# Kernel tuning notes

Hardware: AMD Instinct MI355X
Metric: run time of the kernel (lower is better)

Reference implementation:

```python
import jax, jax.numpy as jnp
import numpy as np

B, S, DIM = 8, 1, 2048
H = 16
QLR, KVLR = 1536, 512
DN, DR, DV = 128, 64, 128      # qk_nope, qk_rope, v head dims
START = 8191                    # start_pos; end_pos = START + S = 8192
EPS = 1e-6
SCALE = (DN + DR) ** -0.5


def _rms(x, w):
    # F.rms_norm: x / sqrt(mean(x^2)+eps) * w
    return x * w * jax.lax.rsqrt(jnp.mean(jnp.square(x), axis=-1, keepdims=True) + EPS)


def _rope(x, cos, sin):
    # x: [..., r]; consecutive pairs (x0,x1) treated as complex, multiplied by cos+i*sin
    xr, xi = x[..., 0::2], x[..., 1::2]
    out_r = xr * cos - xi * sin
    out_i = xr * sin + xi * cos
    return jnp.stack([out_r, out_i], axis=-1).reshape(x.shape)


def setup_inputs() -> dict:
    key = jax.random.key(0)
    ks = jax.random.split(key, 12)
    # rotary tables for the single decode position
    inv_freq = 1.0 / (10000.0 ** (np.arange(0, DR, 2, dtype=np.float32) / DR))  # [DR/2]
    pos = np.arange(START, START + S, dtype=np.float32)[:, None]                # [S,1]
    ang = pos * inv_freq[None, :]                                               # [S, DR/2]
    return {
        "x": jax.random.normal(ks[0], (B, S, DIM), jnp.float32),
        "start_pos": START,
        "freqs_cos": jnp.asarray(np.cos(ang)),
        "freqs_sin": jnp.asarray(np.sin(ang)),
        "kv_cache_prefix": jax.random.normal(ks[1], (B, START, KVLR), jnp.float32),
        "pe_cache_prefix": jax.random.normal(ks[2], (B, START, DR), jnp.float32),
        "wq_a_w": jax.random.normal(ks[3], (QLR, DIM), jnp.float32) * 0.02,
        "wq_a_b": jnp.zeros((QLR,), jnp.float32),
        "q_norm_w": jnp.ones((QLR,), jnp.float32),
        "wq_b_w": jax.random.normal(ks[4], (H * (DN + DR), QLR), jnp.float32) * 0.02,
        "wq_b_b": jnp.zeros((H * (DN + DR),), jnp.float32),
        "wkv_a_w": jax.random.normal(ks[5], (KVLR + DR, DIM), jnp.float32) * 0.02,
        "wkv_a_b": jnp.zeros((KVLR + DR,), jnp.float32),
        "kv_norm_w": jnp.ones((KVLR,), jnp.float32),
        "wkv_b_w": jax.random.normal(ks[6], (H * (DN + DV), KVLR), jnp.float32) * 0.02,
        "wo_w": jax.random.normal(ks[7], (DIM, H * DV), jnp.float32) * 0.02,
        "wo_b": jnp.zeros((DIM,), jnp.float32),
    }


def reference(x, start_pos, freqs_cos, freqs_sin, kv_cache_prefix, pe_cache_prefix,
              wq_a_w, wq_a_b, q_norm_w, wq_b_w, wq_b_b,
              wkv_a_w, wkv_a_b, kv_norm_w, wkv_b_w, wo_w, wo_b):
    b, s, _ = x.shape
    # low-rank query projection
    q = _rms(x @ wq_a_w.T + wq_a_b, q_norm_w) @ wq_b_w.T + wq_b_b
    q = q.reshape(b, s, H, DN + DR)
    q_nope, q_pe = q[..., :DN], q[..., DN:]
    cos = freqs_cos[None, :, None, :]  # [1,s,1,DR/2]
    sin = freqs_sin[None, :, None, :]
    q_pe = _rope(q_pe, cos, sin)
    # compressed KV + rope key branch
    kvpe = x @ wkv_a_w.T + wkv_a_b               # [b,s,KVLR+DR]
    kv, k_pe = kvpe[..., :KVLR], kvpe[..., KVLR:]
    k_pe = _rope(k_pe[:, :, None, :], cos, sin)[:, :, 0, :]
    # weight absorption: project q_nope into latent space through wkv_b's K-part
    wkv_b = wkv_b_w.reshape(H, DN + DV, KVLR)
    q_abs = jnp.einsum('bshd,hdc->bshc', q_nope, wkv_b[:, :DN])
    # append current step to caches
    kv_cache = jnp.concatenate([kv_cache_prefix, _rms(kv, kv_norm_w)], axis=1)  # [b,t,KVLR]
    pe_cache = jnp.concatenate([pe_cache_prefix, k_pe], axis=1)                 # [b,t,DR]
    # attention in latent space (seqlen=1 decode -> no causal mask needed)
    scores = (jnp.einsum('bshc,btc->bsht', q_abs, kv_cache)
              + jnp.einsum('bshr,btr->bsht', q_pe, pe_cache)) * SCALE
    attn = jax.nn.softmax(scores.astype(jnp.float32), axis=-1).astype(x.dtype)
    out = jnp.einsum('bsht,btc->bshc', attn, kv_cache)
    out = jnp.einsum('bshc,hdc->bshd', out, wkv_b[:, DN:])  # V-part of wkv_b
    return out.reshape(b, s, H * DV) @ wo_w.T + wo_b
```

## Files before the change

### kernel.cpp

```cpp
#include <hip/hip_runtime.h>
#include <math.h>

namespace {
constexpr int B_   = 8;
constexpr int DIM_ = 2048;
constexpr int H_   = 16;
constexpr int QLR_ = 1536;
constexpr int KVLR_= 512;
constexpr int DN_  = 128;
constexpr int DR_  = 64;
constexpr int DV_  = 128;
constexpr int TPRE_= 8191;
constexpr int CE_  = 576;
constexpr int NCH_ = 32;
constexpr int CT_  = 256;
constexpr float EPS_ = 1e-6f;
constexpr float SCALE_ = 0.07216878364870322f;
constexpr int SSTR_ = 20;

constexpr size_t WS_QLAT  = 0;
constexpr size_t WS_KVPE  = WS_QLAT  + (size_t)B_*QLR_;
constexpr size_t WS_KVNEW = WS_KVPE  + (size_t)B_*CE_;
constexpr size_t WS_PENEW = WS_KVNEW + (size_t)B_*KVLR_;
constexpr size_t WS_QRS   = WS_PENEW + (size_t)B_*DR_;
constexpr size_t WS_QNOPE = WS_QRS   + (size_t)B_;
constexpr size_t WS_QT    = WS_QNOPE + (size_t)B_*H_*DN_;
constexpr size_t WS_MLOC  = WS_QT    + (size_t)B_*CE_*H_;
constexpr size_t WS_LLOC  = WS_MLOC  + (size_t)B_*H_*NCH_;
constexpr size_t WS_OUT2  = WS_LLOC  + (size_t)B_*H_*NCH_;
constexpr size_t WS_OPART = WS_OUT2  + (size_t)B_*DIM_;
}

__global__ __launch_bounds__(256) void mla_k1(const float* __restrict__ x,
                                              const float* __restrict__ wqa,
                                              const float* __restrict__ bqa,
                                              const float* __restrict__ wkva,
                                              const float* __restrict__ bkva,
                                              float* __restrict__ ws) {
  const int w = threadIdx.x >> 6, l = threadIdx.x & 63;
  const int r = blockIdx.x * 4 + w;
  const float* W; const float* bias; float* out; int rr; int ostride;
  if (r < QLR_) { W = wqa;  bias = bqa;  out = ws + WS_QLAT; rr = r;        ostride = QLR_; }
  else          { W = wkva; bias = bkva; out = ws + WS_KVPE; rr = r - QLR_; ostride = CE_;  }
  const float4* wp = (const float4*)(W + (size_t)rr * DIM_);
  const float4* x4 = (const float4*)x;
  float4 wv[8];
#pragma unroll
  for (int j = 0; j < 8; ++j) wv[j] = wp[l + 64 * j];
  float acc[B_];
#pragma unroll
  for (int b = 0; b < B_; ++b) acc[b] = 0.f;
#pragma unroll
  for (int b = 0; b < B_; ++b) {
#pragma unroll
    for (int j = 0; j < 8; ++j) {
      const float4 xv = x4[b * (DIM_ / 4) + l + 64 * j];
      acc[b] = fmaf(wv[j].x, xv.x, fmaf(wv[j].y, xv.y, fmaf(wv[j].z, xv.z, fmaf(wv[j].w, xv.w, acc[b]))));
    }
  }
#pragma unroll
  for (int b = 0; b < B_; ++b)
#pragma unroll
    for (int s = 32; s; s >>= 1) acc[b] += __shfl_xor(acc[b], s);
  if (l == 0) {
    const float b0 = bias[rr];
#pragma unroll
    for (int b = 0; b < B_; ++b) out[b * ostride + rr] = acc[b] + b0;
  }
}

__global__ __launch_bounds__(256) void mla_k2(const float* __restrict__ kvnw,
                                              const float* __restrict__ fcos,
                                              const float* __restrict__ fsin,
                                              float* __restrict__ ws) {
  const int tid = threadIdx.x;
  const int b = tid >> 5, i = tid & 31;
  const float* kvpe = ws + WS_KVPE + b * CE_;
  float ss = 0.f;
#pragma unroll
  for (int j = 0; j < KVLR_ / 32; ++j) { const float v = kvpe[i + 32 * j]; ss = fmaf(v, v, ss); }
#pragma unroll
  for (int s = 16; s; s >>= 1) ss += __shfl_xor(ss, s, 32);
  const float scale = 1.0f / sqrtf(ss / (float)KVLR_ + EPS_);
  float* kvn = ws + WS_KVNEW + b * KVLR_;
#pragma unroll
  for (int j = 0; j < KVLR_ / 32; ++j) {
    const int c = i + 32 * j;
    kvn[c] = kvpe[c] * kvnw[c] * scale;
  }
  {
    const float xr = kvpe[KVLR_ + 2 * i], xi = kvpe[KVLR_ + 2 * i + 1];
    const float c = fcos[i], s = fsin[i];
    float* pen = ws + WS_PENEW + b * DR_;
    pen[2 * i]     = xr * c - xi * s;
    pen[2 * i + 1] = xr * s + xi * c;
  }
  {
    const float* p = ws + WS_QLAT + b * QLR_;
    float sq = 0.f;
#pragma unroll
    for (int j = 0; j < QLR_ / 32; ++j) { const float v = p[i + 32 * j]; sq = fmaf(v, v, sq); }
#pragma unroll
    for (int s = 16; s; s >>= 1) sq += __shfl_xor(sq, s, 32);
    if (i == 0) ws[WS_QRS + b] = 1.0f / sqrtf(sq / (float)QLR_ + EPS_);
  }
}

__global__ __launch_bounds__(256) void mla_k3(const float* __restrict__ qnw,
                                              const float* __restrict__ wqb,
                                              const float* __restrict__ bqb,
                                              const float* __restrict__ fcos,
                                              const float* __restrict__ fsin,
                                              float* __restrict__ ws) {
  const int w = threadIdx.x >> 6, l = threadIdx.x & 63;
  const int r0 = blockIdx.x * 8 + w * 2;
  const float4* w0p = (const float4*)(wqb + (size_t)r0 * QLR_);
  const float4* w1p = (const float4*)(wqb + (size_t)(r0 + 1) * QLR_);
  const float4* g4  = (const float4*)qnw;
  const float4* x4  = (const float4*)(ws + WS_QLAT);
  float4 wg0[6], wg1[6];
#pragma unroll
  for (int j = 0; j < 6; ++j) {
    const int c4 = l + 64 * j;
    const float4 a = w0p[c4], bb = w1p[c4], g = g4[c4];
    wg0[j].x = a.x * g.x; wg0[j].y = a.y * g.y; wg0[j].z = a.z * g.z; wg0[j].w = a.w * g.w;
    wg1[j].x = bb.x * g.x; wg1[j].y = bb.y * g.y; wg1[j].z = bb.z * g.z; wg1[j].w = bb.w * g.w;
  }
  float acc0[B_], acc1[B_];
#pragma unroll
  for (int b = 0; b < B_; ++b) { acc0[b] = 0.f; acc1[b] = 0.f; }
#pragma unroll
  for (int b = 0; b < B_; ++b) {
#pragma unroll
    for (int j = 0; j < 6; ++j) {
      const float4 xv = x4[b * (QLR_ / 4) + l + 64 * j];
      acc0[b] = fmaf(wg0[j].x, xv.x, fmaf(wg0[j].y, xv.y, fmaf(wg0[j].z, xv.z, fmaf(wg0[j].w, xv.w, acc0[b]))));
      acc1[b] = fmaf(wg1[j].x, xv.x, fmaf(wg1[j].y, xv.y, fmaf(wg1[j].z, xv.z, fmaf(wg1[j].w, xv.w, acc1[b]))));
    }
  }
#pragma unroll
  for (int b = 0; b < B_; ++b)
#pragma unroll
    for (int s = 32; s; s >>= 1) {
      acc0[b] += __shfl_xor(acc0[b], s);
      acc1[b] += __shfl_xor(acc1[b], s);
    }
  if (l == 0) {
    const int h = r0 / (DN_ + DR_);
    const int j0 = r0 - h * (DN_ + DR_);
    const float b0 = bqb[r0], b1 = bqb[r0 + 1];
    if (j0 < DN_) {
      float* qn = ws + WS_QNOPE;
#pragma unroll
      for (int b = 0; b < B_; ++b) {
        const float sb = ws[WS_QRS + b];
        qn[(b * H_ + h) * DN_ + j0]     = acc0[b] * sb + b0;
        qn[(b * H_ + h) * DN_ + j0 + 1] = acc1[b] * sb + b1;
      }
    } else {
      const int i = (j0 - DN_) >> 1;
      const float c = fcos[i], s = fsin[i];
      float* qT = ws + WS_QT;
#pragma unroll
      for (int b = 0; b < B_; ++b) {
        const float sb = ws[WS_QRS + b];
        const float xr = acc0[b] * sb + b0, xi = acc1[b] * sb + b1;
        qT[((size_t)b * CE_ + KVLR_ + 2 * i) * H_ + h]     = xr * c - xi * s;
        qT[((size_t)b * CE_ + KVLR_ + 2 * i + 1) * H_ + h] = xr * s + xi * c;
      }
    }
  }
}

__global__ __launch_bounds__(256) void mla_k4(const float* __restrict__ wkvb,
                                              float* __restrict__ ws) {
  __shared__ float red[7 * 32 * B_];
  const int h = blockIdx.y;
  const int strip = blockIdx.x;
  const int tid = threadIdx.x;
  const int c = tid & 31, dg = tid >> 5;
  const int cg = strip * 32 + c;
  const float* qn = ws + WS_QNOPE;
  float acc[B_];
#pragma unroll
  for (int b = 0; b < B_; ++b) acc[b] = 0.f;
  const float* wp = wkvb + (size_t)h * 256 * KVLR_ + cg;
#pragma unroll
  for (int dd = 0; dd < 16; ++dd) {
    const int d = dg * 16 + dd;
    const float wv = wp[(size_t)d * KVLR_];
#pragma unroll
    for (int b = 0; b < B_; ++b) acc[b] = fmaf(qn[(b * H_ + h) * DN_ + d], wv, acc[b]);
  }
  if (dg > 0) {
#pragma unroll
    for (int b = 0; b < B_; ++b) red[(((dg - 1) * 32) + c) * B_ + b] = acc[b];
  }
  __syncthreads();
  if (dg == 0) {
    float* qT = ws + WS_QT;
#pragma unroll
    for (int b = 0; b < B_; ++b) {
      float v = acc[b];
#pragma unroll
      for (int g = 0; g < 7; ++g) v += red[(g * 32 + c) * B_ + b];
      qT[((size_t)b * CE_ + cg) * H_ + h] = v;
    }
  }
}

__global__ __launch_bounds__(256) void mla_k5(const float* __restrict__ kvpre,
                                              const float* __restrict__ pepre,
                                              float* __restrict__ ws) {
  __shared__ float sl[CT_ * SSTR_];
  const int b = blockIdx.y;
  const int chunk = blockIdx.x;
  const int t0 = chunk * CT_;
  const int tid = threadIdx.x;
  const int w = tid >> 6, l = tid & 63;
  const float* kvnew = ws + WS_KVNEW;
  const float* penew = ws + WS_PENEW;

  {
    const int t = t0 + (w << 6) + l;
    const float* kvrow; const float* perow;
    if (t < TPRE_) {
      kvrow = kvpre + ((size_t)b * TPRE_ + t) * KVLR_;
      perow = pepre + ((size_t)b * TPRE_ + t) * DR_;
    } else {
      kvrow = kvnew + b * KVLR_;
      perow = penew + b * DR_;
    }
    const float* qTb = ws + WS_QT + (size_t)b * CE_ * H_;
    float acc[H_];
#pragma unroll
    for (int h = 0; h < H_; ++h) acc[h] = 0.f;
    auto fma4 = [&](const float4 k, const float* qc) {
#pragma unroll
      for (int h = 0; h < H_; ++h) {
        acc[h] = fmaf(qc[h],          k.x, acc[h]);
        acc[h] = fmaf(qc[H_ + h],     k.y, acc[h]);
        acc[h] = fmaf(qc[2 * H_ + h], k.z, acc[h]);
        acc[h] = fmaf(qc[3 * H_ + h], k.w, acc[h]);
      }
    };
    for (int c16 = 0; c16 < KVLR_; c16 += 16) {
      const float4 k0 = *(const float4*)(kvrow + c16);
      const float4 k1 = *(const float4*)(kvrow + c16 + 4);
      const float4 k2 = *(const float4*)(kvrow + c16 + 8);
      const float4 k3 = *(const float4*)(kvrow + c16 + 12);
      const float* qc = qTb + (size_t)c16 * H_;
      fma4(k0, qc);
      fma4(k1, qc + 4 * H_);
      fma4(k2, qc + 8 * H_);
      fma4(k3, qc + 12 * H_);
    }
    {
      const float4 k0 = *(const float4*)(perow);
      const float4 k1 = *(const float4*)(perow + 4);
      const float4 k2 = *(const float4*)(perow + 8);
      const float4 k3 = *(const float4*)(perow + 12);
      const float4 k4 = *(const float4*)(perow + 16);
      const float4 k5 = *(const float4*)(perow + 20);
      const float4 k6 = *(const float4*)(perow + 24);
      const float4 k7 = *(const float4*)(perow + 28);
      const float* qc = qTb + (size_t)KVLR_ * H_;
      fma4(k0, qc);            fma4(k1, qc + 4 * H_);
      fma4(k2, qc + 8 * H_);   fma4(k3, qc + 12 * H_);
      fma4(k4, qc + 16 * H_);  fma4(k5, qc + 20 * H_);
      fma4(k6, qc + 24 * H_);  fma4(k7, qc + 28 * H_);
      const float4 k8 = *(const float4*)(perow + 32);
      const float4 k9 = *(const float4*)(perow + 36);
      const float4 ka = *(const float4*)(perow + 40);
      const float4 kb = *(const float4*)(perow + 44);
      const float4 kc = *(const float4*)(perow + 48);
      const float4 kd = *(const float4*)(perow + 52);
      const float4 ke = *(const float4*)(perow + 56);
      const float4 kf = *(const float4*)(perow + 60);
      fma4(k8, qc + 32 * H_);  fma4(k9, qc + 36 * H_);
      fma4(ka, qc + 40 * H_);  fma4(kb, qc + 44 * H_);
      fma4(kc, qc + 48 * H_);  fma4(kd, qc + 52 * H_);
      fma4(ke, qc + 56 * H_);  fma4(kf, qc + 60 * H_);
    }
    const int tl = (w << 6) + l;
#pragma unroll
    for (int g = 0; g < 4; ++g) {
      float4 v;
      v.x = acc[4 * g] * SCALE_; v.y = acc[4 * g + 1] * SCALE_;
      v.z = acc[4 * g + 2] * SCALE_; v.w = acc[4 * g + 3] * SCALE_;
      *(float4*)(sl + tl * SSTR_ + 4 * g) = v;
    }
  }
  __syncthreads();

  {
    const int h2 = tid >> 4, grp = tid & 15;
    float m = -3.4e38f;
#pragma unroll
    for (int j = 0; j < 16; ++j) m = fmaxf(m, sl[(grp + 16 * j) * SSTR_ + h2]);
#pragma unroll
    for (int s = 8; s; s >>= 1) m = fmaxf(m, __shfl_xor(m, s, 16));
    float lsum = 0.f;
#pragma unroll
    for (int j = 0; j < 16; ++j) {
      const int idx = (grp + 16 * j) * SSTR_ + h2;
      const float p = __expf(sl[idx] - m);
      sl[idx] = p;
      lsum += p;
    }
#pragma unroll
    for (int s = 8; s; s >>= 1) lsum += __shfl_xor(lsum, s, 16);
    if (grp == 0) {
      ws[WS_MLOC + (b * H_ + h2) * NCH_ + chunk] = m;
      ws[WS_LLOC + (b * H_ + h2) * NCH_ + chunk] = lsum;
    }
  }
  __syncthreads();

  {
    float o[4][8];
#pragma unroll
    for (int a = 0; a < 4; ++a)
#pragma unroll
      for (int j = 0; j < 8; ++j) o[a][j] = 0.f;
    const int hb = w * 4;
    const float* kvb = kvpre + (size_t)b * TPRE_ * KVLR_;
    auto step = [&](const float* kr, int t) {
      const float4 p = *(const float4*)(sl + t * SSTR_ + hb);
#pragma unroll
      for (int j = 0; j < 4; ++j) {
        const float2 kv = *(const float2*)(kr + j * 128 + 2 * l);
        o[0][2 * j]     = fmaf(p.x, kv.x, o[0][2 * j]);
        o[0][2 * j + 1] = fmaf(p.x, kv.y, o[0][2 * j + 1]);
        o[1][2 * j]     = fmaf(p.y, kv.x, o[1][2 * j]);
        o[1][2 * j + 1] = fmaf(p.y, kv.y, o[1][2 * j + 1]);
        o[2][2 * j]     = fmaf(p.z, kv.x, o[2][2 * j]);
        o[2][2 * j + 1] = fmaf(p.z, kv.y, o[2][2 * j + 1]);
        o[3][2 * j]     = fmaf(p.w, kv.x, o[3][2 * j]);
        o[3][2 * j + 1] = fmaf(p.w, kv.y, o[3][2 * j + 1]);
      }
    };
    if (t0 + CT_ <= TPRE_) {
#pragma unroll 4
      for (int t = 0; t < CT_; ++t) step(kvb + (size_t)(t0 + t) * KVLR_, t);
    } else {
      const float* kvn = kvnew + b * KVLR_;
      for (int t = 0; t < CT_; ++t) {
        const float* kr = (t0 + t < TPRE_) ? (kvb + (size_t)(t0 + t) * KVLR_) : kvn;
        step(kr, t);
      }
    }
    float* Op = ws + WS_OPART;
#pragma unroll
    for (int a = 0; a < 4; ++a) {
#pragma unroll
      for (int j = 0; j < 4; ++j) {
        float2 v; v.x = o[a][2 * j]; v.y = o[a][2 * j + 1];
        *(float2*)(Op + (((size_t)(b * H_ + hb + a) * NCH_ + chunk) * KVLR_) + j * 128 + 2 * l) = v;
      }
    }
  }
}

__global__ __launch_bounds__(256) void mla_k6(const float* __restrict__ wkvb,
                                              float* __restrict__ ws) {
  const int h = blockIdx.x, b = blockIdx.y;
  __shared__ float wgt[NCH_];
  __shared__ float ao[KVLR_];
  __shared__ float Linv;
  const int tid = threadIdx.x;
  if (tid < NCH_) {
    const float m = ws[WS_MLOC + (b * H_ + h) * NCH_ + tid];
    float M = m;
#pragma unroll
    for (int s = 16; s; s >>= 1) M = fmaxf(M, __shfl_xor(M, s, 32));
    const float wv = __expf(m - M);
    wgt[tid] = wv;
    float lv = ws[WS_LLOC + (b * H_ + h) * NCH_ + tid] * wv;
#pragma unroll
    for (int s = 16; s; s >>= 1) lv += __shfl_xor(lv, s, 32);
    if (tid == 0) Linv = 1.0f / lv;
  }
  __syncthreads();
  const float* Ob = ws + WS_OPART + (size_t)(b * H_ + h) * NCH_ * KVLR_;
  float s0 = 0.f, s1 = 0.f;
#pragma unroll 4
  for (int i = 0; i < NCH_; ++i) {
    const float wv = wgt[i];
    s0 = fmaf(wv, Ob[(size_t)i * KVLR_ + tid], s0);
    s1 = fmaf(wv, Ob[(size_t)i * KVLR_ + tid + 256], s1);
  }
  const float li = Linv;
  ao[tid] = s0 * li;
  ao[tid + 256] = s1 * li;
  __syncthreads();
  const int v = tid >> 1, half = tid & 1;
  const float* w2 = wkvb + ((size_t)h * 256 + DN_ + v) * KVLR_ + half * 256;
  const float* a = ao + half * 256;
  float s = 0.f;
#pragma unroll
  for (int c = 0; c < 256; c += 4) {
    const float4 wv = *(const float4*)(w2 + c);
    s = fmaf(wv.x, a[c], s);
    s = fmaf(wv.y, a[c + 1], s);
    s = fmaf(wv.z, a[c + 2], s);
    s = fmaf(wv.w, a[c + 3], s);
  }
  s += __shfl_xor(s, 1);
  if (half == 0) ws[WS_OUT2 + b * DIM_ + h * DV_ + v] = s;
}

__global__ __launch_bounds__(256) void mla_k7(const float* __restrict__ wo,
                                              const float* __restrict__ wob,
                                              const float* __restrict__ ws,
                                              float* __restrict__ out) {
  const int w = threadIdx.x >> 6, l = threadIdx.x & 63;
  const int r = blockIdx.x * 4 + w;
  const float4* wp = (const float4*)(wo + (size_t)r * DIM_);
  const float4* x4 = (const float4*)(ws + WS_OUT2);
  float4 wv[8];
#pragma unroll
  for (int j = 0; j < 8; ++j) wv[j] = wp[l + 64 * j];
  float acc[B_];
#pragma unroll
  for (int b = 0; b < B_; ++b) acc[b] = 0.f;
#pragma unroll
  for (int b = 0; b < B_; ++b) {
#pragma unroll
    for (int j = 0; j < 8; ++j) {
      const float4 xv = x4[b * (DIM_ / 4) + l + 64 * j];
      acc[b] = fmaf(wv[j].x, xv.x, fmaf(wv[j].y, xv.y, fmaf(wv[j].z, xv.z, fmaf(wv[j].w, xv.w, acc[b]))));
    }
  }
#pragma unroll
  for (int b = 0; b < B_; ++b)
#pragma unroll
    for (int s = 32; s; s >>= 1) acc[b] += __shfl_xor(acc[b], s);
  if (l == 0) {
    const float b0 = wob[r];
#pragma unroll
    for (int b = 0; b < B_; ++b) out[b * DIM_ + r] = acc[b] + b0;
  }
}

extern "C" void kernel_launch(void* const* d_in, const int* in_sizes, int n_in,
                              void* d_out, int out_size, void* d_ws, size_t ws_size,
                              hipStream_t stream) {
  (void)in_sizes; (void)n_in; (void)out_size; (void)ws_size;
  const float* x     = (const float*)d_in[0];
  const float* fcos  = (const float*)d_in[2];
  const float* fsin  = (const float*)d_in[3];
  const float* kvpre = (const float*)d_in[4];
  const float* pepre = (const float*)d_in[5];
  const float* wqa   = (const float*)d_in[6];
  const float* bqa   = (const float*)d_in[7];
  const float* qnw   = (const float*)d_in[8];
  const float* wqb   = (const float*)d_in[9];
  const float* bqb   = (const float*)d_in[10];
  const float* wkva  = (const float*)d_in[11];
  const float* bkva  = (const float*)d_in[12];
  const float* kvnw  = (const float*)d_in[13];
  const float* wkvb  = (const float*)d_in[14];
  const float* wo    = (const float*)d_in[15];
  const float* wob   = (const float*)d_in[16];
  float* ws  = (float*)d_ws;
  float* out = (float*)d_out;

  mla_k1<<<dim3((QLR_ + CE_) / 4), dim3(256), 0, stream>>>(x, wqa, bqa, wkva, bkva, ws);
  mla_k2<<<dim3(1), dim3(256), 0, stream>>>(kvnw, fcos, fsin, ws);
  mla_k3<<<dim3(H_ * (DN_ + DR_) / 8), dim3(256), 0, stream>>>(qnw, wqb, bqb, fcos, fsin, ws);
  mla_k4<<<dim3(16, H_), dim3(256), 0, stream>>>(wkvb, ws);
  mla_k5<<<dim3(NCH_, B_), dim3(256), 0, stream>>>(kvpre, pepre, ws);
  mla_k6<<<dim3(H_, B_), dim3(256), 0, stream>>>(wkvb, ws);
  mla_k7<<<dim3(DIM_ / 4), dim3(256), 0, stream>>>(wo, wob, ws, out);
}
```

Measured before the change: 408.8 us.

## Split attention chunks smaller and parallelize score dot-products across four warps

Chunk count doubles to 64 with 128 tokens each, and mla_k5 moves to 512 threads. Four wave-pairs each compute a slice of the 576-wide score dot product per token, and the partial sums are reduced through shared memory. Each wave now accumulates two heads in the PV stage instead of four. The goal is more blocks and more parallelism per token, giving better occupancy and latency hiding on the bandwidth-bound cache scan. The cost is extra shared-memory traffic, one more barrier, and twice the partial-output writes and reads in mla_k6.

```diff
diff --git a/kernel.cpp b/kernel.cpp
--- a/kernel.cpp
+++ b/kernel.cpp
@@ -12,8 +12,8 @@
 constexpr int DV_  = 128;
 constexpr int TPRE_= 8191;
 constexpr int CE_  = 576;
-constexpr int NCH_ = 32;
-constexpr int CT_  = 256;
+constexpr int NCH_ = 64;
+constexpr int CT_  = 128;
 constexpr float EPS_ = 1e-6f;
 constexpr float SCALE_ = 0.07216878364870322f;
 constexpr int SSTR_ = 20;
@@ -209,9 +209,10 @@
   }
 }
 
-__global__ __launch_bounds__(256) void mla_k5(const float* __restrict__ kvpre,
-                                              const float* __restrict__ pepre,
-                                              float* __restrict__ ws) {
+__global__ __launch_bounds__(512, 4) void mla_k5(const float* __restrict__ kvpre,
+                                                 const float* __restrict__ pepre,
+                                                 float* __restrict__ ws) {
+  __shared__ float part[4 * CT_ * SSTR_];
   __shared__ float sl[CT_ * SSTR_];
   const int b = blockIdx.y;
   const int chunk = blockIdx.x;
@@ -222,7 +223,9 @@
   const float* penew = ws + WS_PENEW;
 
   {
-    const int t = t0 + (w << 6) + l;
+    const int q4 = w >> 1;
+    const int tl = ((w & 1) << 6) + l;
+    const int t = t0 + tl;
     const float* kvrow; const float* perow;
     if (t < TPRE_) {
       kvrow = kvpre + ((size_t)b * TPRE_ + t) * KVLR_;
@@ -244,72 +247,88 @@
         acc[h] = fmaf(qc[3 * H_ + h], k.w, acc[h]);
       }
     };
-    for (int c16 = 0; c16 < KVLR_; c16 += 16) {
-      const float4 k0 = *(const float4*)(kvrow + c16);
-      const float4 k1 = *(const float4*)(kvrow + c16 + 4);
-      const float4 k2 = *(const float4*)(kvrow + c16 + 8);
-      const float4 k3 = *(const float4*)(kvrow + c16 + 12);
-      const float* qc = qTb + (size_t)c16 * H_;
-      fma4(k0, qc);
-      fma4(k1, qc + 4 * H_);
-      fma4(k2, qc + 8 * H_);
-      fma4(k3, qc + 12 * H_);
-    }
-    {
-      const float4 k0 = *(const float4*)(perow);
-      const float4 k1 = *(const float4*)(perow + 4);
-      const float4 k2 = *(const float4*)(perow + 8);
-      const float4 k3 = *(const float4*)(perow + 12);
-      const float4 k4 = *(const float4*)(perow + 16);
-      const float4 k5 = *(const float4*)(perow + 20);
-      const float4 k6 = *(const float4*)(perow + 24);
-      const float4 k7 = *(const float4*)(perow + 28);
-      const float* qc = qTb + (size_t)KVLR_ * H_;
-      fma4(k0, qc);            fma4(k1, qc + 4 * H_);
-      fma4(k2, qc + 8 * H_);   fma4(k3, qc + 12 * H_);
-      fma4(k4, qc + 16 * H_);  fma4(k5, qc + 20 * H_);
-      fma4(k6, qc + 24 * H_);  fma4(k7, qc + 28 * H_);
-      const float4 k8 = *(const float4*)(perow + 32);
-      const float4 k9 = *(const float4*)(perow + 36);
-      const float4 ka = *(const float4*)(perow + 40);
-      const float4 kb = *(const float4*)(perow + 44);
-      const float4 kc = *(const float4*)(perow + 48);
-      const float4 kd = *(const float4*)(perow + 52);
-      const float4 ke = *(const float4*)(perow + 56);
-      const float4 kf = *(const float4*)(perow + 60);
-      fma4(k8, qc + 32 * H_);  fma4(k9, qc + 36 * H_);
-      fma4(ka, qc + 40 * H_);  fma4(kb, qc + 44 * H_);
-      fma4(kc, qc + 48 * H_);  fma4(kd, qc + 52 * H_);
-      fma4(ke, qc + 56 * H_);  fma4(kf, qc + 60 * H_);
-    }
-    const int tl = (w << 6) + l;
+    if (q4 < 3) {
+      const int cbase = q4 * 144;
+#pragma unroll
+      for (int c16 = 0; c16 < 144; c16 += 16) {
+        const float4 k0 = *(const float4*)(kvrow + cbase + c16);
+        const float4 k1 = *(const float4*)(kvrow + cbase + c16 + 4);
+        const float4 k2 = *(const float4*)(kvrow + cbase + c16 + 8);
+        const float4 k3 = *(const float4*)(kvrow + cbase + c16 + 12);
+        const float* qc = qTb + (size_t)(cbase + c16) * H_;
+        fma4(k0, qc);
+        fma4(k1, qc + 4 * H_);
+        fma4(k2, qc + 8 * H_);
+        fma4(k3, qc + 12 * H_);
+      }
+    } else {
+#pragma unroll
+      for (int c16 = 432; c16 < 512; c16 += 16) {
+        const float4 k0 = *(const float4*)(kvrow + c16);
+        const float4 k1 = *(const float4*)(kvrow + c16 + 4);
+        const float4 k2 = *(const float4*)(kvrow + c16 + 8);
+        const float4 k3 = *(const float4*)(kvrow + c16 + 12);
+        const float* qc = qTb + (size_t)c16 * H_;
+        fma4(k0, qc);
+        fma4(k1, qc + 4 * H_);
+        fma4(k2, qc + 8 * H_);
+        fma4(k3, qc + 12 * H_);
+      }
+#pragma unroll
+      for (int c16 = 0; c16 < 64; c16 += 16) {
+        const float4 k0 = *(const float4*)(perow + c16);
+        const float4 k1 = *(const float4*)(perow + c16 + 4);
+        const float4 k2 = *(const float4*)(perow + c16 + 8);
+        const float4 k3 = *(const float4*)(perow + c16 + 12);
+        const float* qc = qTb + (size_t)(KVLR_ + c16) * H_;
+        fma4(k0, qc);
+        fma4(k1, qc + 4 * H_);
+        fma4(k2, qc + 8 * H_);
+        fma4(k3, qc + 12 * H_);
+      }
+    }
+    float* pp = part + (size_t)(q4 * CT_ + tl) * SSTR_;
 #pragma unroll
     for (int g = 0; g < 4; ++g) {
       float4 v;
-      v.x = acc[4 * g] * SCALE_; v.y = acc[4 * g + 1] * SCALE_;
-      v.z = acc[4 * g + 2] * SCALE_; v.w = acc[4 * g + 3] * SCALE_;
-      *(float4*)(sl + tl * SSTR_ + 4 * g) = v;
-    }
-  }
-  __syncthreads();
-
-  {
-    const int h2 = tid >> 4, grp = tid & 15;
+      v.x = acc[4 * g]; v.y = acc[4 * g + 1];
+      v.z = acc[4 * g + 2]; v.w = acc[4 * g + 3];
+      *(float4*)(pp + 4 * g) = v;
+    }
+  }
+  __syncthreads();
+
+  {
+#pragma unroll
+    for (int k = 0; k < (CT_ * H_) / 512; ++k) {
+      const int idx = tid + 512 * k;
+      const int t = idx >> 4, h = idx & 15;
+      const float v = part[(0 * CT_ + t) * SSTR_ + h]
+                    + part[(1 * CT_ + t) * SSTR_ + h]
+                    + part[(2 * CT_ + t) * SSTR_ + h]
+                    + part[(3 * CT_ + t) * SSTR_ + h];
+      sl[t * SSTR_ + h] = v * SCALE_;
+    }
+  }
+  __syncthreads();
+
+  {
+    const int h2 = tid >> 5, grp = tid & 31;
     float m = -3.4e38f;
 #pragma unroll
-    for (int j = 0; j < 16; ++j) m = fmaxf(m, sl[(grp + 16 * j) * SSTR_ + h2]);
-#pragma unroll
-    for (int s = 8; s; s >>= 1) m = fmaxf(m, __shfl_xor(m, s, 16));
+    for (int j = 0; j < CT_ / 32; ++j) m = fmaxf(m, sl[(grp + 32 * j) * SSTR_ + h2]);
+#pragma unroll
+    for (int s = 16; s; s >>= 1) m = fmaxf(m, __shfl_xor(m, s, 32));
     float lsum = 0.f;
 #pragma unroll
-    for (int j = 0; j < 16; ++j) {
-      const int idx = (grp + 16 * j) * SSTR_ + h2;
+    for (int j = 0; j < CT_ / 32; ++j) {
+      const int idx = (grp + 32 * j) * SSTR_ + h2;
       const float p = __expf(sl[idx] - m);
       sl[idx] = p;
       lsum += p;
     }
 #pragma unroll
-    for (int s = 8; s; s >>= 1) lsum += __shfl_xor(lsum, s, 16);
+    for (int s = 16; s; s >>= 1) lsum += __shfl_xor(lsum, s, 32);
     if (grp == 0) {
       ws[WS_MLOC + (b * H_ + h2) * NCH_ + chunk] = m;
       ws[WS_LLOC + (b * H_ + h2) * NCH_ + chunk] = lsum;
@@ -318,15 +337,15 @@
   __syncthreads();
 
   {
-    float o[4][8];
-#pragma unroll
-    for (int a = 0; a < 4; ++a)
+    float o[2][8];
+#pragma unroll
+    for (int a = 0; a < 2; ++a)
 #pragma unroll
       for (int j = 0; j < 8; ++j) o[a][j] = 0.f;
-    const int hb = w * 4;
+    const int hb = w * 2;
     const float* kvb = kvpre + (size_t)b * TPRE_ * KVLR_;
     auto step = [&](const float* kr, int t) {
-      const float4 p = *(const float4*)(sl + t * SSTR_ + hb);
+      const float2 p = *(const float2*)(sl + t * SSTR_ + hb);
 #pragma unroll
       for (int j = 0; j < 4; ++j) {
         const float2 kv = *(const float2*)(kr + j * 128 + 2 * l);
@@ -334,10 +353,6 @@
         o[0][2 * j + 1] = fmaf(p.x, kv.y, o[0][2 * j + 1]);
         o[1][2 * j]     = fmaf(p.y, kv.x, o[1][2 * j]);
         o[1][2 * j + 1] = fmaf(p.y, kv.y, o[1][2 * j + 1]);
-        o[2][2 * j]     = fmaf(p.z, kv.x, o[2][2 * j]);
-        o[2][2 * j + 1] = fmaf(p.z, kv.y, o[2][2 * j + 1]);
-        o[3][2 * j]     = fmaf(p.w, kv.x, o[3][2 * j]);
-        o[3][2 * j + 1] = fmaf(p.w, kv.y, o[3][2 * j + 1]);
       }
     };
     if (t0 + CT_ <= TPRE_) {
@@ -352,7 +367,7 @@
     }
     float* Op = ws + WS_OPART;
 #pragma unroll
-    for (int a = 0; a < 4; ++a) {
+    for (int a = 0; a < 2; ++a) {
 #pragma unroll
       for (int j = 0; j < 4; ++j) {
         float2 v; v.x = o[a][2 * j]; v.y = o[a][2 * j + 1];
@@ -373,12 +388,12 @@
     const float m = ws[WS_MLOC + (b * H_ + h) * NCH_ + tid];
     float M = m;
 #pragma unroll
-    for (int s = 16; s; s >>= 1) M = fmaxf(M, __shfl_xor(M, s, 32));
+    for (int s = 32; s; s >>= 1) M = fmaxf(M, __shfl_xor(M, s));
     const float wv = __expf(m - M);
     wgt[tid] = wv;
     float lv = ws[WS_LLOC + (b * H_ + h) * NCH_ + tid] * wv;
 #pragma unroll
-    for (int s = 16; s; s >>= 1) lv += __shfl_xor(lv, s, 32);
+    for (int s = 32; s; s >>= 1) lv += __shfl_xor(lv, s);
     if (tid == 0) Linv = 1.0f / lv;
   }
   __syncthreads();
@@ -470,7 +485,7 @@
   mla_k2<<<dim3(1), dim3(256), 0, stream>>>(kvnw, fcos, fsin, ws);
   mla_k3<<<dim3(H_ * (DN_ + DR_) / 8), dim3(256), 0, stream>>>(qnw, wqb, bqb, fcos, fsin, ws);
   mla_k4<<<dim3(16, H_), dim3(256), 0, stream>>>(wkvb, ws);
-  mla_k5<<<dim3(NCH_, B_), dim3(256), 0, stream>>>(kvpre, pepre, ws);
+  mla_k5<<<dim3(NCH_, B_), dim3(512), 0, stream>>>(kvpre, pepre, ws);
   mla_k6<<<dim3(H_, B_), dim3(256), 0, stream>>>(wkvb, ws);
   mla_k7<<<dim3(DIM_ / 4), dim3(256), 0, stream>>>(wo, wob, ws, out);
 }
```

After: 443.6 us. 1.09x slower.

## Stage KV tiles in LDS with online softmax in attention kernel

Applied to the files above, without the earlier changes.

Restructures the attention kernel so each 512-thread block loads 32-token tiles of the KV and PE caches into shared memory, using coalesced float4 loads with register prefetch of the next tile. Scores, an online-softmax update and the P·V accumulation are all computed from LDS, so the KV cache is read from global memory once instead of twice. The transposed q vectors are also staged in LDS. In exchange there are more barriers per tile and a larger LDS footprint, which may limit occupancy.

```diff
diff --git a/kernel.cpp b/kernel.cpp
--- a/kernel.cpp
+++ b/kernel.cpp
@@ -14,9 +14,11 @@
 constexpr int CE_  = 576;
 constexpr int NCH_ = 32;
 constexpr int CT_  = 256;
+constexpr int TS_  = 32;
+constexpr int RS_  = 580;
+constexpr int PSTR_= 20;
 constexpr float EPS_ = 1e-6f;
 constexpr float SCALE_ = 0.07216878364870322f;
-constexpr int SSTR_ = 20;
 
 constexpr size_t WS_QLAT  = 0;
 constexpr size_t WS_KVPE  = WS_QLAT  + (size_t)B_*QLR_;
@@ -209,155 +211,151 @@
   }
 }
 
-__global__ __launch_bounds__(256) void mla_k5(const float* __restrict__ kvpre,
-                                              const float* __restrict__ pepre,
-                                              float* __restrict__ ws) {
-  __shared__ float sl[CT_ * SSTR_];
+__global__ __launch_bounds__(512, 2) void mla_k5(const float* __restrict__ kvpre,
+                                                 const float* __restrict__ pepre,
+                                                 float* __restrict__ ws) {
+  __shared__ float kv_lds[TS_ * RS_];
+  __shared__ float q_lds[H_ * RS_];
+  __shared__ float p_lds[TS_ * PSTR_];
+  __shared__ float m_st[H_], l_st[H_], f_st[H_];
+
   const int b = blockIdx.y;
   const int chunk = blockIdx.x;
   const int t0 = chunk * CT_;
   const int tid = threadIdx.x;
-  const int w = tid >> 6, l = tid & 63;
-  const float* kvnew = ws + WS_KVNEW;
-  const float* penew = ws + WS_PENEW;
 
   {
-    const int t = t0 + (w << 6) + l;
-    const float* kvrow; const float* perow;
-    if (t < TPRE_) {
-      kvrow = kvpre + ((size_t)b * TPRE_ + t) * KVLR_;
-      perow = pepre + ((size_t)b * TPRE_ + t) * DR_;
-    } else {
-      kvrow = kvnew + b * KVLR_;
-      perow = penew + b * DR_;
-    }
-    const float* qTb = ws + WS_QT + (size_t)b * CE_ * H_;
-    float acc[H_];
-#pragma unroll
-    for (int h = 0; h < H_; ++h) acc[h] = 0.f;
-    auto fma4 = [&](const float4 k, const float* qc) {
-#pragma unroll
-      for (int h = 0; h < H_; ++h) {
-        acc[h] = fmaf(qc[h],          k.x, acc[h]);
-        acc[h] = fmaf(qc[H_ + h],     k.y, acc[h]);
-        acc[h] = fmaf(qc[2 * H_ + h], k.z, acc[h]);
-        acc[h] = fmaf(qc[3 * H_ + h], k.w, acc[h]);
-      }
-    };
-    for (int c16 = 0; c16 < KVLR_; c16 += 16) {
-      const float4 k0 = *(const float4*)(kvrow + c16);
-      const float4 k1 = *(const float4*)(kvrow + c16 + 4);
-      const float4 k2 = *(const float4*)(kvrow + c16 + 8);
-      const float4 k3 = *(const float4*)(kvrow + c16 + 12);
-      const float* qc = qTb + (size_t)c16 * H_;
-      fma4(k0, qc);
-      fma4(k1, qc + 4 * H_);
-      fma4(k2, qc + 8 * H_);
-      fma4(k3, qc + 12 * H_);
-    }
+    const float4* qsrc = (const float4*)(ws + WS_QT + (size_t)b * CE_ * H_);
+#pragma unroll
+    for (int it = 0; it < 5; ++it) {
+      const int idx = tid + 512 * it;
+      if (idx < (CE_ * H_) / 4) {
+        const float4 v = qsrc[idx];
+        const int c = idx >> 2, h4 = (idx & 3) * 4;
+        q_lds[(h4 + 0) * RS_ + c] = v.x;
+        q_lds[(h4 + 1) * RS_ + c] = v.y;
+        q_lds[(h4 + 2) * RS_ + c] = v.z;
+        q_lds[(h4 + 3) * RS_ + c] = v.w;
+      }
+    }
+    if (tid < H_) { m_st[tid] = -3.4e38f; l_st[tid] = 0.f; }
+  }
+
+  int fr[9], fw[9];
+#pragma unroll
+  for (int i = 0; i < 9; ++i) {
+    const int f = tid + 512 * i;
+    fr[i] = f / 144; fw[i] = f % 144;
+  }
+  const float* kvnew = ws + WS_KVNEW + b * KVLR_;
+  const float* penew = ws + WS_PENEW + b * DR_;
+
+  float4 stg[9];
+  auto loadR = [&](int ts) {
+#pragma unroll
+    for (int i = 0; i < 9; ++i) {
+      const int t = t0 + ts * TS_ + fr[i];
+      const int wi = fw[i];
+      const float* src;
+      if (t < TPRE_) {
+        src = (wi < 128) ? (kvpre + ((size_t)b * TPRE_ + t) * KVLR_ + wi * 4)
+                         : (pepre + ((size_t)b * TPRE_ + t) * DR_ + (wi - 128) * 4);
+      } else {
+        src = (wi < 128) ? (kvnew + wi * 4) : (penew + (wi - 128) * 4);
+      }
+      stg[i] = *(const float4*)src;
+    }
+  };
+  loadR(0);
+
+  float o[H_];
+#pragma unroll
+  for (int h = 0; h < H_; ++h) o[h] = 0.f;
+
+  const int t_sc = tid >> 4, h_sc = tid & 15;
+  const int h2 = tid >> 5, tg = tid & 31;
+
+  for (int ts = 0; ts < CT_ / TS_; ++ts) {
+    __syncthreads();
+#pragma unroll
+    for (int i = 0; i < 9; ++i)
+      *(float4*)(kv_lds + fr[i] * RS_ + fw[i] * 4) = stg[i];
+    if (ts + 1 < CT_ / TS_) loadR(ts + 1);
+    __syncthreads();
+
     {
-      const float4 k0 = *(const float4*)(perow);
-      const float4 k1 = *(const float4*)(perow + 4);
-      const float4 k2 = *(const float4*)(perow + 8);
-      const float4 k3 = *(const float4*)(perow + 12);
-      const float4 k4 = *(const float4*)(perow + 16);
-      const float4 k5 = *(const float4*)(perow + 20);
-      const float4 k6 = *(const float4*)(perow + 24);
-      const float4 k7 = *(const float4*)(perow + 28);
-      const float* qc = qTb + (size_t)KVLR_ * H_;
-      fma4(k0, qc);            fma4(k1, qc + 4 * H_);
-      fma4(k2, qc + 8 * H_);   fma4(k3, qc + 12 * H_);
-      fma4(k4, qc + 16 * H_);  fma4(k5, qc + 20 * H_);
-      fma4(k6, qc + 24 * H_);  fma4(k7, qc + 28 * H_);
-      const float4 k8 = *(const float4*)(perow + 32);
-      const float4 k9 = *(const float4*)(perow + 36);
-      const float4 ka = *(const float4*)(perow + 40);
-      const float4 kb = *(const float4*)(perow + 44);
-      const float4 kc = *(const float4*)(perow + 48);
-      const float4 kd = *(const float4*)(perow + 52);
-      const float4 ke = *(const float4*)(perow + 56);
-      const float4 kf = *(const float4*)(perow + 60);
-      fma4(k8, qc + 32 * H_);  fma4(k9, qc + 36 * H_);
-      fma4(ka, qc + 40 * H_);  fma4(kb, qc + 44 * H_);
-      fma4(kc, qc + 48 * H_);  fma4(kd, qc + 52 * H_);
-      fma4(ke, qc + 56 * H_);  fma4(kf, qc + 60 * H_);
-    }
-    const int tl = (w << 6) + l;
-#pragma unroll
-    for (int g = 0; g < 4; ++g) {
-      float4 v;
-      v.x = acc[4 * g] * SCALE_; v.y = acc[4 * g + 1] * SCALE_;
-      v.z = acc[4 * g + 2] * SCALE_; v.w = acc[4 * g + 3] * SCALE_;
-      *(float4*)(sl + tl * SSTR_ + 4 * g) = v;
-    }
-  }
-  __syncthreads();
+      const float4* kr = (const float4*)(kv_lds + t_sc * RS_);
+      const float4* qr = (const float4*)(q_lds + h_sc * RS_);
+      float ax = 0.f, ay = 0.f, az = 0.f, aw = 0.f;
+#pragma unroll
+      for (int c4 = 0; c4 < 144; ++c4) {
+        const float4 k = kr[c4], q = qr[c4];
+        ax = fmaf(k.x, q.x, ax); ay = fmaf(k.y, q.y, ay);
+        az = fmaf(k.z, q.z, az); aw = fmaf(k.w, q.w, aw);
+      }
+      p_lds[t_sc * PSTR_ + h_sc] = (ax + ay + az + aw) * SCALE_;
+    }
+    __syncthreads();
+
+    {
+      const float s = p_lds[tg * PSTR_ + h2];
+      float msub = s;
+#pragma unroll
+      for (int d = 16; d; d >>= 1) msub = fmaxf(msub, __shfl_xor(msub, d, 32));
+      const float mold = m_st[h2];
+      const float mnew = fmaxf(mold, msub);
+      const float e = __expf(s - mnew);
+      float lsum = e;
+#pragma unroll
+      for (int d = 16; d; d >>= 1) lsum += __shfl_xor(lsum, d, 32);
+      p_lds[tg * PSTR_ + h2] = e;
+      if (tg == 0) {
+        const float fac = __expf(mold - mnew);
+        f_st[h2] = fac;
+        l_st[h2] = l_st[h2] * fac + lsum;
+        m_st[h2] = mnew;
+      }
+    }
+    __syncthreads();
+
+    {
+      const int c = tid;
+      const float4 f0 = *(const float4*)&f_st[0];
+      const float4 f1 = *(const float4*)&f_st[4];
+      const float4 f2 = *(const float4*)&f_st[8];
+      const float4 f3 = *(const float4*)&f_st[12];
+      o[0] *= f0.x; o[1] *= f0.y; o[2] *= f0.z; o[3] *= f0.w;
+      o[4] *= f1.x; o[5] *= f1.y; o[6] *= f1.z; o[7] *= f1.w;
+      o[8] *= f2.x; o[9] *= f2.y; o[10] *= f2.z; o[11] *= f2.w;
+      o[12] *= f3.x; o[13] *= f3.y; o[14] *= f3.z; o[15] *= f3.w;
+#pragma unroll 8
+      for (int t = 0; t < TS_; ++t) {
+        const float kvv = kv_lds[t * RS_ + c];
+        const float4 p0 = *(const float4*)(p_lds + t * PSTR_);
+        const float4 p1 = *(const float4*)(p_lds + t * PSTR_ + 4);
+        const float4 p2 = *(const float4*)(p_lds + t * PSTR_ + 8);
+        const float4 p3 = *(const float4*)(p_lds + t * PSTR_ + 12);
+        o[0]  = fmaf(p0.x, kvv, o[0]);  o[1]  = fmaf(p0.y, kvv, o[1]);
+        o[2]  = fmaf(p0.z, kvv, o[2]);  o[3]  = fmaf(p0.w, kvv, o[3]);
+        o[4]  = fmaf(p1.x, kvv, o[4]);  o[5]  = fmaf(p1.y, kvv, o[5]);
+        o[6]  = fmaf(p1.z, kvv, o[6]);  o[7]  = fmaf(p1.w, kvv, o[7]);
+        o[8]  = fmaf(p2.x, kvv, o[8]);  o[9]  = fmaf(p2.y, kvv, o[9]);
+        o[10] = fmaf(p2.z, kvv, o[10]); o[11] = fmaf(p2.w, kvv, o[11]);
+        o[12] = fmaf(p3.x, kvv, o[12]); o[13] = fmaf(p3.y, kvv, o[13]);
+        o[14] = fmaf(p3.z, kvv, o[14]); o[15] = fmaf(p3.w, kvv, o[15]);
+      }
+    }
+  }
 
   {
-    const int h2 = tid >> 4, grp = tid & 15;
-    float m = -3.4e38f;
-#pragma unroll
-    for (int j = 0; j < 16; ++j) m = fmaxf(m, sl[(grp + 16 * j) * SSTR_ + h2]);
-#pragma unroll
-    for (int s = 8; s; s >>= 1) m = fmaxf(m, __shfl_xor(m, s, 16));
-    float lsum = 0.f;
-#pragma unroll
-    for (int j = 0; j < 16; ++j) {
-      const int idx = (grp + 16 * j) * SSTR_ + h2;
-      const float p = __expf(sl[idx] - m);
-      sl[idx] = p;
-      lsum += p;
-    }
-#pragma unroll
-    for (int s = 8; s; s >>= 1) lsum += __shfl_xor(lsum, s, 16);
-    if (grp == 0) {
-      ws[WS_MLOC + (b * H_ + h2) * NCH_ + chunk] = m;
-      ws[WS_LLOC + (b * H_ + h2) * NCH_ + chunk] = lsum;
-    }
-  }
-  __syncthreads();
-
-  {
-    float o[4][8];
-#pragma unroll
-    for (int a = 0; a < 4; ++a)
-#pragma unroll
-      for (int j = 0; j < 8; ++j) o[a][j] = 0.f;
-    const int hb = w * 4;
-    const float* kvb = kvpre + (size_t)b * TPRE_ * KVLR_;
-    auto step = [&](const float* kr, int t) {
-      const float4 p = *(const float4*)(sl + t * SSTR_ + hb);
-#pragma unroll
-      for (int j = 0; j < 4; ++j) {
-        const float2 kv = *(const float2*)(kr + j * 128 + 2 * l);
-        o[0][2 * j]     = fmaf(p.x, kv.x, o[0][2 * j]);
-        o[0][2 * j + 1] = fmaf(p.x, kv.y, o[0][2 * j + 1]);
-        o[1][2 * j]     = fmaf(p.y, kv.x, o[1][2 * j]);
-        o[1][2 * j + 1] = fmaf(p.y, kv.y, o[1][2 * j + 1]);
-        o[2][2 * j]     = fmaf(p.z, kv.x, o[2][2 * j]);
-        o[2][2 * j + 1] = fmaf(p.z, kv.y, o[2][2 * j + 1]);
-        o[3][2 * j]     = fmaf(p.w, kv.x, o[3][2 * j]);
-        o[3][2 * j + 1] = fmaf(p.w, kv.y, o[3][2 * j + 1]);
-      }
-    };
-    if (t0 + CT_ <= TPRE_) {
-#pragma unroll 4
-      for (int t = 0; t < CT_; ++t) step(kvb + (size_t)(t0 + t) * KVLR_, t);
-    } else {
-      const float* kvn = kvnew + b * KVLR_;
-      for (int t = 0; t < CT_; ++t) {
-        const float* kr = (t0 + t < TPRE_) ? (kvb + (size_t)(t0 + t) * KVLR_) : kvn;
-        step(kr, t);
-      }
-    }
-    float* Op = ws + WS_OPART;
-#pragma unroll
-    for (int a = 0; a < 4; ++a) {
-#pragma unroll
-      for (int j = 0; j < 4; ++j) {
-        float2 v; v.x = o[a][2 * j]; v.y = o[a][2 * j + 1];
-        *(float2*)(Op + (((size_t)(b * H_ + hb + a) * NCH_ + chunk) * KVLR_) + j * 128 + 2 * l) = v;
-      }
+    const int c = tid;
+    float* Op = ws + WS_OPART + ((size_t)(b * H_) * NCH_ + chunk) * KVLR_;
+#pragma unroll
+    for (int h = 0; h < H_; ++h)
+      Op[(size_t)h * NCH_ * KVLR_ + c] = o[h];
+    if (tid < H_) {
+      ws[WS_MLOC + (b * H_ + tid) * NCH_ + chunk] = m_st[tid];
+      ws[WS_LLOC + (b * H_ + tid) * NCH_ + chunk] = l_st[tid];
     }
   }
 }
@@ -470,7 +468,7 @@
   mla_k2<<<dim3(1), dim3(256), 0, stream>>>(kvnw, fcos, fsin, ws);
   mla_k3<<<dim3(H_ * (DN_ + DR_) / 8), dim3(256), 0, stream>>>(qnw, wqb, bqb, fcos, fsin, ws);
   mla_k4<<<dim3(16, H_), dim3(256), 0, stream>>>(wkvb, ws);
-  mla_k5<<<dim3(NCH_, B_), dim3(256), 0, stream>>>(kvpre, pepre, ws);
+  mla_k5<<<dim3(NCH_, B_), dim3(512), 0, stream>>>(kvpre, pepre, ws);
   mla_k6<<<dim3(H_, B_), dim3(256), 0, stream>>>(wkvb, ws);
   mla_k7<<<dim3(DIM_ / 4), dim3(256), 0, stream>>>(wo, wob, ws, out);
 }
```

New measurement: 426.6 us. 1.04x slower.
